# Performance work log

Hardware: AMD Instinct MI355X
Metric: run time of the kernel (lower is better)

The kernel has to match this reference:

```python
import jax, jax.numpy as jnp
import numpy as np

N_NODES = 100000
N_EDGES = 1600000
D_IN, D_HID, D_OUT = 64, 64, 32


def _glorot(key, shape):
    fan_in = shape[0]
    return jax.random.normal(key, shape, dtype=jnp.float32) / np.sqrt(fan_in)


def setup_inputs() -> dict:
    key = jax.random.key(0)
    ks = jax.random.split(key, 12)
    x = jax.random.normal(ks[0], (N_NODES, D_IN), dtype=jnp.float32)
    edge_index = jax.random.randint(ks[1], (2, N_EDGES), 0, N_NODES, dtype=jnp.int32)
    dims = [(D_IN, D_HID), (D_HID, D_HID), (D_HID, D_OUT)]
    params = {}
    for i, (din, dout) in enumerate(dims):
        params[f"Wl{i}"] = _glorot(ks[2 + 3 * i], (din, dout))
        params[f"Wr{i}"] = _glorot(ks[3 + 3 * i], (din, dout))
        params[f"b{i}"] = jnp.zeros((dout,), dtype=jnp.float32)
    return {"x": x, "edge_index": edge_index, **params}


def _sage_conv(h, src, dst, deg_inv, Wl, Wr, b):
    # mean-aggregate neighbor features: gather from src, scatter-sum to dst
    msg_sum = jax.ops.segment_sum(h[src], dst, num_segments=N_NODES)  # [N, F]
    mean = msg_sum * deg_inv[:, None]
    # lin_l(mean) + bias + lin_r(h)  (PyG SAGEConv: bias lives in lin_l)
    return mean @ Wl + b + h @ Wr


def reference(x, edge_index, Wl0, Wr0, b0, Wl1, Wr1, b1, Wl2, Wr2, b2):
    src, dst = edge_index[0], edge_index[1]
    deg = jax.ops.segment_sum(jnp.ones((N_EDGES,), x.dtype), dst, num_segments=N_NODES)
    deg_inv = 1.0 / jnp.maximum(deg, 1.0)  # mean with clamp for isolated nodes
    h = jax.nn.elu(_sage_conv(x, src, dst, deg_inv, Wl0, Wr0, b0))
    h = jax.nn.elu(_sage_conv(h, src, dst, deg_inv, Wl1, Wr1, b1))
    return _sage_conv(h, src, dst, deg_inv, Wl2, Wr2, b2)
```

## Files before the change

### kernel.cpp

```cpp
#include <hip/hip_runtime.h>
#include <cstdint>
#include <cstddef>


constexpr int SBW = 256;
constexpr int LOGSBW = 8;
constexpr int CAPS = 4608;
constexpr int CAPSP = 5632;
constexpr int CHK = 2048;

typedef __attribute__((ext_vector_type(8))) short s16x8;
typedef __attribute__((ext_vector_type(4))) float f32x4;
typedef __attribute__((ext_vector_type(2))) float f32x2;
typedef __attribute__((ext_vector_type(4))) int i32x4;

__device__ inline unsigned short f2bf(float f) {
  unsigned u = __builtin_bit_cast(unsigned, f);
  u += 0x7FFFu + ((u >> 16) & 1u);
  return (unsigned short)(u >> 16);
}
__device__ inline float bf2f(unsigned short b) {
  unsigned u = ((unsigned)b) << 16;
  return __builtin_bit_cast(float, u);
}
__device__ inline unsigned char f2fp8(float f) {
  int p = __builtin_amdgcn_cvt_pk_fp8_f32(f, f, 0, false);
  return (unsigned char)(p & 0xFF);
}


__global__ __launch_bounds__(256) void init_ws(int* __restrict__ bcur, int NSB,
                                               const float* __restrict__ Wl0,
                                               const float* __restrict__ Wr0,
                                               const float* __restrict__ Wl1,
                                               const float* __restrict__ Wr1,
                                               const float* __restrict__ Wl2,
                                               const float* __restrict__ Wr2,
                                               unsigned short* __restrict__ Wsw) {
  const int tid = threadIdx.x;
  if (blockIdx.x == 0) {
    for (int i = tid; i < NSB; i += 256) bcur[i] = 0;
    return;
  }
  int g = (blockIdx.x - 1) * 256 + tid;
  if (g >= 10240) return;
  int s = g * 2;
  int layer, off;
  if (s < 8192)       { layer = 0; off = 0; }
  else if (s < 16384) { layer = 1; off = 8192; }
  else                { layer = 2; off = 16384; }
  int t = s - off;
  int D = (layer == 2) ? 32 : 64;
  int NTT = D / 16;
  int tt = t >> 10;
  int rem = t & 1023;
  int plane = rem >> 9;
  int rem2 = rem & 511;
  int lane = rem2 >> 3;
  int j = rem2 & 7;
  int q = lane >> 4, m = lane & 15;
  int k = plane * 32 + q * 8 + j;
  const float* W;
  int c;
  if (tt < NTT) {
    c = tt;
    W = (layer == 0) ? Wl0 : (layer == 1) ? Wl1 : Wl2;
  } else {
    c = tt - NTT;
    W = (layer == 0) ? Wr0 : (layer == 1) ? Wr1 : Wr2;
  }
  int col = c * 16 + m;
  unsigned lo = f2bf(W[k * D + col]);
  unsigned hi = f2bf(W[(k + 1) * D + col]);
  *(unsigned*)&Wsw[s] = lo | (hi << 16);
}


__global__ __launch_bounds__(256) void bin_coarse(const int* __restrict__ src,
                                                  const int* __restrict__ dst,
                                                  int* __restrict__ bcur,
                                                  unsigned int* __restrict__ coarse,
                                                  int NSB, int E) {
  __shared__ int h[512];
  __shared__ unsigned ed[CHK];
  __shared__ short sb[CHK];
  const int tid = threadIdx.x;
  for (int i = tid; i < NSB; i += 256) h[i] = 0;
  __syncthreads();
  const int e0 = blockIdx.x * CHK;
  const int e1 = min(E, e0 + CHK);
  for (int e = e0 + tid; e < e1; e += 256) {
    int d = dst[e];
    int s = src[e];
    int b = d >> LOGSBW;
    ed[e - e0] = (unsigned)s | ((unsigned)(d & (SBW - 1)) << 17);
    sb[e - e0] = (short)b;
    atomicAdd(&h[b], 1);
  }
  __syncthreads();
  for (int i = tid; i < NSB; i += 256) {
    int c = h[i];
    h[i] = c ? (i * CAPS + atomicAdd(&bcur[i], c)) : 0;
  }
  __syncthreads();
  const int n = e1 - e0;
  for (int k = tid; k < n; k += 256) {
    int b = sb[k];
    int pos = atomicAdd(&h[b], 1);
    if (pos < (b + 1) * CAPS)
      coarse[pos] = ed[k];
  }
}


__global__ __launch_bounds__(256) void csr_gemm0(const unsigned int* __restrict__ coarse,
                                                 const int* __restrict__ bcur,
                                                 int* __restrict__ rowstart,
                                                 int* __restrict__ degarr,
                                                 float* __restrict__ deg_inv,
                                                 int* __restrict__ colidx,
                                                 const float* __restrict__ x,
                                                 const unsigned short* __restrict__ Wf,
                                                 const float* __restrict__ bias,
                                                 unsigned char* __restrict__ t_out,
                                                 unsigned short* __restrict__ r_out,
                                                 int N, int NSB) {
  __shared__ int cnt[SBW];
  __shared__ int sc[SBW];
  __shared__ int cur[SBW];
  const int tid = threadIdx.x;
  if ((int)blockIdx.x < NSB) {
    const int b = blockIdx.x;
    cnt[tid] = 0;
    __syncthreads();
    const int ec = min(bcur[b], CAPS);
    const int baseC = b * CAPS;
    const int baseP = b * CAPSP;
    for (int e = tid; e < ec; e += 256)
      atomicAdd(&cnt[coarse[baseC + e] >> 17], 1);
    __syncthreads();
    int v = cnt[tid];
    int pc = (v + 3) & ~3;
    sc[tid] = pc;
    __syncthreads();
    for (int off = 1; off < SBW; off <<= 1) {
      int y = sc[tid];
      if (tid >= off) y += sc[tid - off];
      __syncthreads();
      sc[tid] = y;
      __syncthreads();
    }
    int pex = sc[tid] - pc;
    cur[tid] = pex;
    int gn = b * SBW + tid;
    if (gn < N) {
      rowstart[gn] = baseP + pex;
      degarr[gn] = pc;
      deg_inv[gn] = 1.0f / (float)(v > 1 ? v : 1);
    }
    __syncthreads();
    for (int e = tid; e < ec; e += 256) {
      unsigned p = coarse[baseC + e];
      int dl = (int)(p >> 17);
      int s = (int)(p & 0x1FFFFu);
      int l = atomicAdd(&cur[dl], 1);
      if (l < CAPSP)
        colidx[baseP + l] = s;
    }
    int pe = pex + pc;
    if (pe > CAPSP) pe = CAPSP;
    for (int l = pex + v; l < pe; ++l) colidx[baseP + l] = N;
    return;
  }
  constexpr int DOUT = 64;
  constexpr int NTT = 4;
  const int gbid = blockIdx.x - NSB;
  if (gbid == 0 && tid < 16)
    ((unsigned*)t_out)[(size_t)N * 16 + tid] = 0u;
  const int wv = tid >> 6, lane = tid & 63;
  const int q = lane >> 4, m = lane & 15;
  const int row = gbid * 64 + wv * 16 + m;
  const int rowc = row < N ? row : N - 1;
  const float* xp = &x[(size_t)rowc * 64];
  float4 f0 = *(const float4*)&xp[q * 8];
  float4 f1 = *(const float4*)&xp[q * 8 + 4];
  float4 f2 = *(const float4*)&xp[32 + q * 8];
  float4 f3 = *(const float4*)&xp[32 + q * 8 + 4];
  s16x8 a0, a1;
  a0[0] = (short)f2bf(f0.x); a0[1] = (short)f2bf(f0.y);
  a0[2] = (short)f2bf(f0.z); a0[3] = (short)f2bf(f0.w);
  a0[4] = (short)f2bf(f1.x); a0[5] = (short)f2bf(f1.y);
  a0[6] = (short)f2bf(f1.z); a0[7] = (short)f2bf(f1.w);
  a1[0] = (short)f2bf(f2.x); a1[1] = (short)f2bf(f2.y);
  a1[2] = (short)f2bf(f2.z); a1[3] = (short)f2bf(f2.w);
  a1[4] = (short)f2bf(f3.x); a1[5] = (short)f2bf(f3.y);
  a1[6] = (short)f2bf(f3.z); a1[7] = (short)f2bf(f3.w);

  f32x4 acc[2 * NTT];
#pragma unroll
  for (int c = 0; c < 2 * NTT; ++c) acc[c] = (f32x4){0.f, 0.f, 0.f, 0.f};
#pragma unroll
  for (int c = 0; c < 2 * NTT; ++c) {
    s16x8 b0 = *(const s16x8*)&Wf[(c * 2 + 0) * 512 + lane * 8];
    s16x8 b1 = *(const s16x8*)&Wf[(c * 2 + 1) * 512 + lane * 8];
    acc[c] = __builtin_amdgcn_mfma_f32_16x16x32_bf16(a0, b0, acc[c], 0, 0, 0);
    acc[c] = __builtin_amdgcn_mfma_f32_16x16x32_bf16(a1, b1, acc[c], 0, 0, 0);
  }

  const int orow = gbid * 64 + wv * 16 + q * 4;
#pragma unroll
  for (int c = 0; c < NTT; ++c) {
#pragma unroll
    for (int i = 0; i < 4; ++i) {
      int r_ = orow + i;
      if (r_ < N) t_out[(size_t)r_ * DOUT + c * 16 + m] = f2fp8(acc[c][i]);
    }
  }
#pragma unroll
  for (int c = 0; c < NTT; ++c) {
    float bv = bias[c * 16 + m];
#pragma unroll
    for (int i = 0; i < 4; ++i) {
      int r_ = orow + i;
      if (r_ < N) r_out[(size_t)r_ * 64 + c * 16 + m] = f2bf(acc[NTT + c][i] + bv);
    }
  }
}


template <int DOUT, bool TFP8, bool RB16>
__global__ __launch_bounds__(256) void gemm_mfma(const unsigned short* __restrict__ Hm,
                                                 const unsigned short* __restrict__ Wf,
                                                 const float* __restrict__ bias,
                                                 void* __restrict__ t_out,
                                                 void* __restrict__ r_out, int N) {
  constexpr int NTT = DOUT / 16;
  constexpr int ROWB = TFP8 ? DOUT : DOUT * 2;
  const int tid = threadIdx.x;
  if (blockIdx.x == 0 && tid < ROWB / 4)
    ((unsigned*)((char*)t_out + (size_t)N * ROWB))[tid] = 0u;
  const int wv = tid >> 6, lane = tid & 63;
  const int q = lane >> 4, m = lane & 15;
  const int row = blockIdx.x * 64 + wv * 16 + m;
  const int rowc = row < N ? row : N - 1;
  const s16x8 a0 = *(const s16x8*)&Hm[(size_t)rowc * 64 + q * 8];
  const s16x8 a1 = *(const s16x8*)&Hm[(size_t)rowc * 64 + 32 + q * 8];

  f32x4 acc[2 * NTT];
#pragma unroll
  for (int c = 0; c < 2 * NTT; ++c) acc[c] = (f32x4){0.f, 0.f, 0.f, 0.f};
#pragma unroll
  for (int c = 0; c < 2 * NTT; ++c) {
    s16x8 b0 = *(const s16x8*)&Wf[(c * 2 + 0) * 512 + lane * 8];
    s16x8 b1 = *(const s16x8*)&Wf[(c * 2 + 1) * 512 + lane * 8];
    acc[c] = __builtin_amdgcn_mfma_f32_16x16x32_bf16(a0, b0, acc[c], 0, 0, 0);
    acc[c] = __builtin_amdgcn_mfma_f32_16x16x32_bf16(a1, b1, acc[c], 0, 0, 0);
  }

  const int orow = blockIdx.x * 64 + wv * 16 + q * 4;
#pragma unroll
  for (int c = 0; c < NTT; ++c) {
#pragma unroll
    for (int i = 0; i < 4; ++i) {
      int r_ = orow + i;
      if (r_ < N) {
        if (TFP8)
          ((unsigned char*)t_out)[(size_t)r_ * DOUT + c * 16 + m] = f2fp8(acc[c][i]);
        else
          ((unsigned short*)t_out)[(size_t)r_ * DOUT + c * 16 + m] = f2bf(acc[c][i]);
      }
    }
  }
#pragma unroll
  for (int c = 0; c < NTT; ++c) {
    float bv = bias[c * 16 + m];
#pragma unroll
    for (int i = 0; i < 4; ++i) {
      int r_ = orow + i;
      if (r_ < N) {
        if (RB16)
          ((unsigned short*)r_out)[(size_t)r_ * DOUT + c * 16 + m] =
              f2bf(acc[NTT + c][i] + bv);
        else
          ((float*)r_out)[(size_t)r_ * DOUT + c * 16 + m] = acc[NTT + c][i] + bv;
      }
    }
  }
}


__global__ __launch_bounds__(256) void gather_fp8(const uint2* __restrict__ t,
                                                  const unsigned short* __restrict__ r,
                                                  const float* __restrict__ deg_inv,
                                                  const int* __restrict__ rowstart,
                                                  const int* __restrict__ degarr,
                                                  const int* __restrict__ colidx,
                                                  unsigned short* __restrict__ Xout,
                                                  int N) {
  int node = blockIdx.x * 32 + (threadIdx.x >> 3);
  int lane = threadIdx.x & 7;
  if (node >= N) return;
  int b = rowstart[node];
  int e = b + degarr[node];
  float s[8];
#pragma unroll
  for (int k = 0; k < 8; ++k) s[k] = 0.f;
  int i = b;
  if (i + 8 <= e) {
    i32x4 c0 = *(const i32x4*)&colidx[i];
    i32x4 c1 = *(const i32x4*)&colidx[i + 4];
    uint2 va[8];
    va[0] = t[(size_t)c0.x * 8 + lane];
    va[1] = t[(size_t)c0.y * 8 + lane];
    va[2] = t[(size_t)c0.z * 8 + lane];
    va[3] = t[(size_t)c0.w * 8 + lane];
    va[4] = t[(size_t)c1.x * 8 + lane];
    va[5] = t[(size_t)c1.y * 8 + lane];
    va[6] = t[(size_t)c1.z * 8 + lane];
    va[7] = t[(size_t)c1.w * 8 + lane];
    while (i + 16 <= e) {
      i32x4 n0 = *(const i32x4*)&colidx[i + 8];
      i32x4 n1 = *(const i32x4*)&colidx[i + 12];
      uint2 vb[8];
      vb[0] = t[(size_t)n0.x * 8 + lane];
      vb[1] = t[(size_t)n0.y * 8 + lane];
      vb[2] = t[(size_t)n0.z * 8 + lane];
      vb[3] = t[(size_t)n0.w * 8 + lane];
      vb[4] = t[(size_t)n1.x * 8 + lane];
      vb[5] = t[(size_t)n1.y * 8 + lane];
      vb[6] = t[(size_t)n1.z * 8 + lane];
      vb[7] = t[(size_t)n1.w * 8 + lane];
#pragma unroll
      for (int j = 0; j < 8; ++j) {
        f32x2 p0 = __builtin_amdgcn_cvt_pk_f32_fp8((int)va[j].x, false);
        f32x2 p1 = __builtin_amdgcn_cvt_pk_f32_fp8((int)va[j].x, true);
        f32x2 p2 = __builtin_amdgcn_cvt_pk_f32_fp8((int)va[j].y, false);
        f32x2 p3 = __builtin_amdgcn_cvt_pk_f32_fp8((int)va[j].y, true);
        s[0] += p0[0]; s[1] += p0[1]; s[2] += p1[0]; s[3] += p1[1];
        s[4] += p2[0]; s[5] += p2[1]; s[6] += p3[0]; s[7] += p3[1];
      }
#pragma unroll
      for (int j = 0; j < 8; ++j) va[j] = vb[j];
      i += 8;
    }
#pragma unroll
    for (int j = 0; j < 8; ++j) {
      f32x2 p0 = __builtin_amdgcn_cvt_pk_f32_fp8((int)va[j].x, false);
      f32x2 p1 = __builtin_amdgcn_cvt_pk_f32_fp8((int)va[j].x, true);
      f32x2 p2 = __builtin_amdgcn_cvt_pk_f32_fp8((int)va[j].y, false);
      f32x2 p3 = __builtin_amdgcn_cvt_pk_f32_fp8((int)va[j].y, true);
      s[0] += p0[0]; s[1] += p0[1]; s[2] += p1[0]; s[3] += p1[1];
      s[4] += p2[0]; s[5] += p2[1]; s[6] += p3[0]; s[7] += p3[1];
    }
    i += 8;
  }
  if (i < e) {
    i32x4 c0 = *(const i32x4*)&colidx[i];
    uint2 v[4];
    v[0] = t[(size_t)c0.x * 8 + lane];
    v[1] = t[(size_t)c0.y * 8 + lane];
    v[2] = t[(size_t)c0.z * 8 + lane];
    v[3] = t[(size_t)c0.w * 8 + lane];
#pragma unroll
    for (int j = 0; j < 4; ++j) {
      f32x2 p0 = __builtin_amdgcn_cvt_pk_f32_fp8((int)v[j].x, false);
      f32x2 p1 = __builtin_amdgcn_cvt_pk_f32_fp8((int)v[j].x, true);
      f32x2 p2 = __builtin_amdgcn_cvt_pk_f32_fp8((int)v[j].y, false);
      f32x2 p3 = __builtin_amdgcn_cvt_pk_f32_fp8((int)v[j].y, true);
      s[0] += p0[0]; s[1] += p0[1]; s[2] += p1[0]; s[3] += p1[1];
      s[4] += p2[0]; s[5] += p2[1]; s[6] += p3[0]; s[7] += p3[1];
    }
  }
  float dv = deg_inv[node];
  const s16x8 rv = *(const s16x8*)&r[(size_t)node * 64 + lane * 8];
  s16x8 hv;
#pragma unroll
  for (int k = 0; k < 8; ++k) {
    float ak = s[k] * dv + bf2f((unsigned short)rv[k]);
    ak = ak > 0.f ? ak : (expf(ak) - 1.f);
    hv[k] = (short)f2bf(ak);
  }
  *(s16x8*)&Xout[(size_t)node * 64 + lane * 8] = hv;
}


__global__ __launch_bounds__(256) void gather_out(const uint2* __restrict__ t,
                                                  const float* __restrict__ r,
                                                  const float* __restrict__ deg_inv,
                                                  const int* __restrict__ rowstart,
                                                  const int* __restrict__ degarr,
                                                  const int* __restrict__ colidx,
                                                  float* __restrict__ out, int N) {
  int node = blockIdx.x * 32 + (threadIdx.x >> 3);
  int lane = threadIdx.x & 7;
  if (node >= N) return;
  int b = rowstart[node];
  int e = b + degarr[node];
  float s0 = 0.f, s1 = 0.f, s2 = 0.f, s3 = 0.f;
  int i = b;
  if (i + 8 <= e) {
    i32x4 c0 = *(const i32x4*)&colidx[i];
    i32x4 c1 = *(const i32x4*)&colidx[i + 4];
    uint2 va[8];
    va[0] = t[(size_t)c0.x * 8 + lane];
    va[1] = t[(size_t)c0.y * 8 + lane];
    va[2] = t[(size_t)c0.z * 8 + lane];
    va[3] = t[(size_t)c0.w * 8 + lane];
    va[4] = t[(size_t)c1.x * 8 + lane];
    va[5] = t[(size_t)c1.y * 8 + lane];
    va[6] = t[(size_t)c1.z * 8 + lane];
    va[7] = t[(size_t)c1.w * 8 + lane];
    while (i + 16 <= e) {
      i32x4 n0 = *(const i32x4*)&colidx[i + 8];
      i32x4 n1 = *(const i32x4*)&colidx[i + 12];
      uint2 vb[8];
      vb[0] = t[(size_t)n0.x * 8 + lane];
      vb[1] = t[(size_t)n0.y * 8 + lane];
      vb[2] = t[(size_t)n0.z * 8 + lane];
      vb[3] = t[(size_t)n0.w * 8 + lane];
      vb[4] = t[(size_t)n1.x * 8 + lane];
      vb[5] = t[(size_t)n1.y * 8 + lane];
      vb[6] = t[(size_t)n1.z * 8 + lane];
      vb[7] = t[(size_t)n1.w * 8 + lane];
#pragma unroll
      for (int j = 0; j < 8; ++j) {
        s0 += bf2f((unsigned short)(va[j].x & 0xFFFFu));
        s1 += bf2f((unsigned short)(va[j].x >> 16));
        s2 += bf2f((unsigned short)(va[j].y & 0xFFFFu));
        s3 += bf2f((unsigned short)(va[j].y >> 16));
      }
#pragma unroll
      for (int j = 0; j < 8; ++j) va[j] = vb[j];
      i += 8;
    }
#pragma unroll
    for (int j = 0; j < 8; ++j) {
      s0 += bf2f((unsigned short)(va[j].x & 0xFFFFu));
      s1 += bf2f((unsigned short)(va[j].x >> 16));
      s2 += bf2f((unsigned short)(va[j].y & 0xFFFFu));
      s3 += bf2f((unsigned short)(va[j].y >> 16));
    }
    i += 8;
  }
  if (i < e) {
    i32x4 c0 = *(const i32x4*)&colidx[i];
    uint2 v[4];
    v[0] = t[(size_t)c0.x * 8 + lane];
    v[1] = t[(size_t)c0.y * 8 + lane];
    v[2] = t[(size_t)c0.z * 8 + lane];
    v[3] = t[(size_t)c0.w * 8 + lane];
#pragma unroll
    for (int j = 0; j < 4; ++j) {
      s0 += bf2f((unsigned short)(v[j].x & 0xFFFFu));
      s1 += bf2f((unsigned short)(v[j].x >> 16));
      s2 += bf2f((unsigned short)(v[j].y & 0xFFFFu));
      s3 += bf2f((unsigned short)(v[j].y >> 16));
    }
  }
  float dv = deg_inv[node];
  float4 rv = *(const float4*)&r[(size_t)node * 32 + 4 * lane];
  *(float4*)&out[(size_t)node * 32 + 4 * lane] =
      make_float4(s0 * dv + rv.x, s1 * dv + rv.y, s2 * dv + rv.z, s3 * dv + rv.w);
}


extern "C" void kernel_launch(void* const* d_in, const int* in_sizes, int n_in,
                              void* d_out, int out_size, void* d_ws, size_t ws_size,
                              hipStream_t stream) {
  const float* x   = (const float*)d_in[0];
  const int*   ei  = (const int*)d_in[1];
  const float* Wl0 = (const float*)d_in[2];
  const float* Wr0 = (const float*)d_in[3];
  const float* b0  = (const float*)d_in[4];
  const float* Wl1 = (const float*)d_in[5];
  const float* Wr1 = (const float*)d_in[6];
  const float* b1  = (const float*)d_in[7];
  const float* Wl2 = (const float*)d_in[8];
  const float* Wr2 = (const float*)d_in[9];
  const float* b2  = (const float*)d_in[10];
  float* out = (float*)d_out;

  const int N = in_sizes[0] / 64;
  const int E = in_sizes[1] / 2;
  const int* srcv = ei;
  const int* dstv = ei + E;
  const int NSB = (N + SBW - 1) >> LOGSBW;

  auto al = [](size_t v) { return (v + 255) & ~(size_t)255; };
  char* w = (char*)d_ws;
  size_t oBcur = 0;
  size_t oRow  = oBcur + al(4 * (size_t)NSB);
  size_t oDeg  = oRow + al(4 * (size_t)N);
  size_t oDinv = oDeg + al(4 * (size_t)N);
  size_t oWsw  = oDinv + al(4 * (size_t)N);
  size_t oBin  = oWsw + al(2 * 20480);
  size_t oCol  = oBin + al(4 * (size_t)NSB * CAPS);
  size_t oP8   = oCol + al(4 * (size_t)NSB * CAPSP);
  size_t oP16  = oP8 + al((size_t)(N + 1) * 64);
  size_t oX    = oP16 + al((size_t)(N + 1) * 64);
  size_t oR    = oX + al(2 * (size_t)N * 64);

  int*            bcur     = (int*)(w + oBcur);
  int*            rowstart = (int*)(w + oRow);
  int*            degarr   = (int*)(w + oDeg);
  float*          deg_inv  = (float*)(w + oDinv);
  unsigned short* Wsw      = (unsigned short*)(w + oWsw);
  unsigned*       coarse   = (unsigned*)(w + oBin);
  int*            colidx   = (int*)(w + oCol);
  unsigned char*  P8       = (unsigned char*)(w + oP8);
  unsigned short* P16      = (unsigned short*)(w + oP16);
  unsigned short* X        = (unsigned short*)(w + oX);
  unsigned short* Rb       = (unsigned short*)(w + oR);
  float*          Rf       = (float*)(w + oR);

  int bbl = (E + CHK - 1) / CHK;
  int gb = (N + 63) / 64;
  int ggb = (N + 31) / 32;

  init_ws<<<41, 256, 0, stream>>>(bcur, NSB, Wl0, Wr0, Wl1, Wr1, Wl2, Wr2, Wsw);
  bin_coarse<<<bbl, 256, 0, stream>>>(srcv, dstv, bcur, coarse, NSB, E);
  csr_gemm0<<<NSB + gb, 256, 0, stream>>>(coarse, bcur, rowstart, degarr,
                                          deg_inv, colidx, x, Wsw, b0, P8, Rb,
                                          N, NSB);
  gather_fp8<<<ggb, 256, 0, stream>>>((const uint2*)P8, Rb, deg_inv, rowstart,
                                      degarr, colidx, X, N);
  gemm_mfma<64, true, true><<<gb, 256, 0, stream>>>(X, Wsw + 8192, b1, P8, Rb, N);
  gather_fp8<<<ggb, 256, 0, stream>>>((const uint2*)P8, Rb, deg_inv, rowstart,
                                      degarr, colidx, X, N);
  gemm_mfma<32, false, false><<<gb, 256, 0, stream>>>(X, Wsw + 16384, b2, P16, Rf, N);
  gather_out<<<ggb, 256, 0, stream>>>((const uint2*)P16, Rf, deg_inv, rowstart,
                                      degarr, colidx, out, N);
}
```

Baseline: 241.8 us.

## Merge weight-swizzle into binning kernel and pack per-node CSR metadata

Folds the weight bf16 swizzle blocks into the edge-binning launch and replaces the bcur init kernel with a memset. The binning kernel now keeps edges in registers instead of shared-memory staging. Row start, padded degree and raw degree are packed into one int2 per node, so each gather does one load and computes the inverse degree inline. The packing assumes degrees fit in 16 bits.

```diff
diff --git a/kernel.cpp b/kernel.cpp
--- a/kernel.cpp
+++ b/kernel.cpp
@@ -29,73 +29,74 @@
 }
 
 
-__global__ __launch_bounds__(256) void init_ws(int* __restrict__ bcur, int NSB,
-                                               const float* __restrict__ Wl0,
-                                               const float* __restrict__ Wr0,
-                                               const float* __restrict__ Wl1,
-                                               const float* __restrict__ Wr1,
-                                               const float* __restrict__ Wl2,
-                                               const float* __restrict__ Wr2,
-                                               unsigned short* __restrict__ Wsw) {
+__global__ __launch_bounds__(256) void bin_stage(const int* __restrict__ src,
+                                                 const int* __restrict__ dst,
+                                                 int* __restrict__ bcur,
+                                                 unsigned int* __restrict__ coarse,
+                                                 int NSB, int E,
+                                                 const float* __restrict__ Wl0,
+                                                 const float* __restrict__ Wr0,
+                                                 const float* __restrict__ Wl1,
+                                                 const float* __restrict__ Wr1,
+                                                 const float* __restrict__ Wl2,
+                                                 const float* __restrict__ Wr2,
+                                                 unsigned short* __restrict__ Wsw) {
+  __shared__ int h[512];
   const int tid = threadIdx.x;
-  if (blockIdx.x == 0) {
-    for (int i = tid; i < NSB; i += 256) bcur[i] = 0;
+  const int bbl = (E + CHK - 1) / CHK;
+  if ((int)blockIdx.x >= bbl) {
+    int g = (blockIdx.x - bbl) * 256 + tid;
+    if (g >= 10240) return;
+    int s = g * 2;
+    int layer, off;
+    if (s < 8192)       { layer = 0; off = 0; }
+    else if (s < 16384) { layer = 1; off = 8192; }
+    else                { layer = 2; off = 16384; }
+    int t = s - off;
+    int D = (layer == 2) ? 32 : 64;
+    int NTT = D / 16;
+    int tt = t >> 10;
+    int rem = t & 1023;
+    int plane = rem >> 9;
+    int rem2 = rem & 511;
+    int lane = rem2 >> 3;
+    int j = rem2 & 7;
+    int q = lane >> 4, m = lane & 15;
+    int k = plane * 32 + q * 8 + j;
+    const float* W;
+    int c;
+    if (tt < NTT) {
+      c = tt;
+      W = (layer == 0) ? Wl0 : (layer == 1) ? Wl1 : Wl2;
+    } else {
+      c = tt - NTT;
+      W = (layer == 0) ? Wr0 : (layer == 1) ? Wr1 : Wr2;
+    }
+    int col = c * 16 + m;
+    unsigned lo = f2bf(W[k * D + col]);
+    unsigned hi = f2bf(W[(k + 1) * D + col]);
+    *(unsigned*)&Wsw[s] = lo | (hi << 16);
     return;
   }
-  int g = (blockIdx.x - 1) * 256 + tid;
-  if (g >= 10240) return;
-  int s = g * 2;
-  int layer, off;
-  if (s < 8192)       { layer = 0; off = 0; }
-  else if (s < 16384) { layer = 1; off = 8192; }
-  else                { layer = 2; off = 16384; }
-  int t = s - off;
-  int D = (layer == 2) ? 32 : 64;
-  int NTT = D / 16;
-  int tt = t >> 10;
-  int rem = t & 1023;
-  int plane = rem >> 9;
-  int rem2 = rem & 511;
-  int lane = rem2 >> 3;
-  int j = rem2 & 7;
-  int q = lane >> 4, m = lane & 15;
-  int k = plane * 32 + q * 8 + j;
-  const float* W;
-  int c;
-  if (tt < NTT) {
-    c = tt;
-    W = (layer == 0) ? Wl0 : (layer == 1) ? Wl1 : Wl2;
-  } else {
-    c = tt - NTT;
-    W = (layer == 0) ? Wr0 : (layer == 1) ? Wr1 : Wr2;
-  }
-  int col = c * 16 + m;
-  unsigned lo = f2bf(W[k * D + col]);
-  unsigned hi = f2bf(W[(k + 1) * D + col]);
-  *(unsigned*)&Wsw[s] = lo | (hi << 16);
-}
-
-
-__global__ __launch_bounds__(256) void bin_coarse(const int* __restrict__ src,
-                                                  const int* __restrict__ dst,
-                                                  int* __restrict__ bcur,
-                                                  unsigned int* __restrict__ coarse,
-                                                  int NSB, int E) {
-  __shared__ int h[512];
-  __shared__ unsigned ed[CHK];
-  __shared__ short sb[CHK];
-  const int tid = threadIdx.x;
   for (int i = tid; i < NSB; i += 256) h[i] = 0;
   __syncthreads();
   const int e0 = blockIdx.x * CHK;
   const int e1 = min(E, e0 + CHK);
-  for (int e = e0 + tid; e < e1; e += 256) {
-    int d = dst[e];
-    int s = src[e];
-    int b = d >> LOGSBW;
-    ed[e - e0] = (unsigned)s | ((unsigned)(d & (SBW - 1)) << 17);
-    sb[e - e0] = (short)b;
-    atomicAdd(&h[b], 1);
+  unsigned pk[8];
+  int bk[8];
+#pragma unroll
+  for (int k = 0; k < 8; ++k) {
+    int e = e0 + tid + k * 256;
+    if (e < e1) {
+      int d = dst[e];
+      int s = src[e];
+      int b = d >> LOGSBW;
+      pk[k] = (unsigned)s | ((unsigned)(d & (SBW - 1)) << 17);
+      bk[k] = b;
+      atomicAdd(&h[b], 1);
+    } else {
+      bk[k] = -1;
+    }
   }
   __syncthreads();
   for (int i = tid; i < NSB; i += 256) {
@@ -103,21 +104,20 @@
     h[i] = c ? (i * CAPS + atomicAdd(&bcur[i], c)) : 0;
   }
   __syncthreads();
-  const int n = e1 - e0;
-  for (int k = tid; k < n; k += 256) {
-    int b = sb[k];
-    int pos = atomicAdd(&h[b], 1);
-    if (pos < (b + 1) * CAPS)
-      coarse[pos] = ed[k];
+#pragma unroll
+  for (int k = 0; k < 8; ++k) {
+    if (bk[k] >= 0) {
+      int pos = atomicAdd(&h[bk[k]], 1);
+      if (pos < (bk[k] + 1) * CAPS)
+        coarse[pos] = pk[k];
+    }
   }
 }
 
 
 __global__ __launch_bounds__(256) void csr_gemm0(const unsigned int* __restrict__ coarse,
                                                  const int* __restrict__ bcur,
-                                                 int* __restrict__ rowstart,
-                                                 int* __restrict__ degarr,
-                                                 float* __restrict__ deg_inv,
+                                                 int2* __restrict__ meta,
                                                  int* __restrict__ colidx,
                                                  const float* __restrict__ x,
                                                  const unsigned short* __restrict__ Wf,
@@ -153,11 +153,8 @@
     int pex = sc[tid] - pc;
     cur[tid] = pex;
     int gn = b * SBW + tid;
-    if (gn < N) {
-      rowstart[gn] = baseP + pex;
-      degarr[gn] = pc;
-      deg_inv[gn] = 1.0f / (float)(v > 1 ? v : 1);
-    }
+    if (gn < N)
+      meta[gn] = make_int2(baseP + pex, pc | (v << 16));
     __syncthreads();
     for (int e = tid; e < ec; e += 256) {
       unsigned p = coarse[baseC + e];
@@ -291,17 +288,18 @@
 
 __global__ __launch_bounds__(256) void gather_fp8(const uint2* __restrict__ t,
                                                   const unsigned short* __restrict__ r,
-                                                  const float* __restrict__ deg_inv,
-                                                  const int* __restrict__ rowstart,
-                                                  const int* __restrict__ degarr,
+                                                  const int2* __restrict__ meta,
                                                   const int* __restrict__ colidx,
                                                   unsigned short* __restrict__ Xout,
                                                   int N) {
   int node = blockIdx.x * 32 + (threadIdx.x >> 3);
   int lane = threadIdx.x & 7;
   if (node >= N) return;
-  int b = rowstart[node];
-  int e = b + degarr[node];
+  const int2 mt = meta[node];
+  const int b = mt.x;
+  const int pc = mt.y & 0xFFFF;
+  const int vr = mt.y >> 16;
+  const int e = b + pc;
   float s[8];
 #pragma unroll
   for (int k = 0; k < 8; ++k) s[k] = 0.f;
@@ -371,7 +369,7 @@
       s[4] += p2[0]; s[5] += p2[1]; s[6] += p3[0]; s[7] += p3[1];
     }
   }
-  float dv = deg_inv[node];
+  const float dv = 1.0f / (float)(vr > 1 ? vr : 1);
   const s16x8 rv = *(const s16x8*)&r[(size_t)node * 64 + lane * 8];
   s16x8 hv;
 #pragma unroll
@@ -386,16 +384,17 @@
 
 __global__ __launch_bounds__(256) void gather_out(const uint2* __restrict__ t,
                                                   const float* __restrict__ r,
-                                                  const float* __restrict__ deg_inv,
-                                                  const int* __restrict__ rowstart,
-                                                  const int* __restrict__ degarr,
+                                                  const int2* __restrict__ meta,
                                                   const int* __restrict__ colidx,
                                                   float* __restrict__ out, int N) {
   int node = blockIdx.x * 32 + (threadIdx.x >> 3);
   int lane = threadIdx.x & 7;
   if (node >= N) return;
-  int b = rowstart[node];
-  int e = b + degarr[node];
+  const int2 mt = meta[node];
+  const int b = mt.x;
+  const int pc = mt.y & 0xFFFF;
+  const int vr = mt.y >> 16;
+  const int e = b + pc;
   float s0 = 0.f, s1 = 0.f, s2 = 0.f, s3 = 0.f;
   int i = b;
   if (i + 8 <= e) {
@@ -457,7 +456,7 @@
       s3 += bf2f((unsigned short)(v[j].y >> 16));
     }
   }
-  float dv = deg_inv[node];
+  const float dv = 1.0f / (float)(vr > 1 ? vr : 1);
   float4 rv = *(const float4*)&r[(size_t)node * 32 + 4 * lane];
   *(float4*)&out[(size_t)node * 32 + 4 * lane] =
       make_float4(s0 * dv + rv.x, s1 * dv + rv.y, s2 * dv + rv.z, s3 * dv + rv.w);
@@ -489,10 +488,8 @@
   auto al = [](size_t v) { return (v + 255) & ~(size_t)255; };
   char* w = (char*)d_ws;
   size_t oBcur = 0;
-  size_t oRow  = oBcur + al(4 * (size_t)NSB);
-  size_t oDeg  = oRow + al(4 * (size_t)N);
-  size_t oDinv = oDeg + al(4 * (size_t)N);
-  size_t oWsw  = oDinv + al(4 * (size_t)N);
+  size_t oMeta = oBcur + al(4 * (size_t)NSB);
+  size_t oWsw  = oMeta + al(8 * (size_t)N);
   size_t oBin  = oWsw + al(2 * 20480);
   size_t oCol  = oBin + al(4 * (size_t)NSB * CAPS);
   size_t oP8   = oCol + al(4 * (size_t)NSB * CAPSP);
@@ -501,9 +498,7 @@
   size_t oR    = oX + al(2 * (size_t)N * 64);
 
   int*            bcur     = (int*)(w + oBcur);
-  int*            rowstart = (int*)(w + oRow);
-  int*            degarr   = (int*)(w + oDeg);
-  float*          deg_inv  = (float*)(w + oDinv);
+  int2*           meta     = (int2*)(w + oMeta);
   unsigned short* Wsw      = (unsigned short*)(w + oWsw);
   unsigned*       coarse   = (unsigned*)(w + oBin);
   int*            colidx   = (int*)(w + oCol);
@@ -517,17 +512,14 @@
   int gb = (N + 63) / 64;
   int ggb = (N + 31) / 32;
 
-  init_ws<<<41, 256, 0, stream>>>(bcur, NSB, Wl0, Wr0, Wl1, Wr1, Wl2, Wr2, Wsw);
-  bin_coarse<<<bbl, 256, 0, stream>>>(srcv, dstv, bcur, coarse, NSB, E);
-  csr_gemm0<<<NSB + gb, 256, 0, stream>>>(coarse, bcur, rowstart, degarr,
-                                          deg_inv, colidx, x, Wsw, b0, P8, Rb,
-                                          N, NSB);
-  gather_fp8<<<ggb, 256, 0, stream>>>((const uint2*)P8, Rb, deg_inv, rowstart,
-                                      degarr, colidx, X, N);
+  hipMemsetAsync(bcur, 0, (size_t)NSB * 4, stream);
+  bin_stage<<<bbl + 40, 256, 0, stream>>>(srcv, dstv, bcur, coarse, NSB, E,
+                                          Wl0, Wr0, Wl1, Wr1, Wl2, Wr2, Wsw);
+  csr_gemm0<<<NSB + gb, 256, 0, stream>>>(coarse, bcur, meta, colidx, x, Wsw,
+                                          b0, P8, Rb, N, NSB);
+  gather_fp8<<<ggb, 256, 0, stream>>>((const uint2*)P8, Rb, meta, colidx, X, N);
   gemm_mfma<64, true, true><<<gb, 256, 0, stream>>>(X, Wsw + 8192, b1, P8, Rb, N);
-  gather_fp8<<<ggb, 256, 0, stream>>>((const uint2*)P8, Rb, deg_inv, rowstart,
-                                      degarr, colidx, X, N);
+  gather_fp8<<<ggb, 256, 0, stream>>>((const uint2*)P8, Rb, meta, colidx, X, N);
   gemm_mfma<32, false, false><<<gb, 256, 0, stream>>>(X, Wsw + 16384, b2, P16, Rf, N);
-  gather_out<<<ggb, 256, 0, stream>>>((const uint2*)P16, Rf, deg_inv, rowstart,
-                                      degarr, colidx, out, N);
-}
+  gather_out<<<ggb, 256, 0, stream>>>((const uint2*)P16, Rf, meta, colidx, out, N);
+}
```

Measured after the change: 241.6 us. About the same (-0.1%).
